# Performance work log

Measured on AMD Instinct MI355X. Metric: run time of the kernel, lower is better.

The kernel has to match this reference:

```python
import jax, jax.numpy as jnp
import numpy as np

SIZE = 1 << 24          # number of leaves (power of two, so bound == SIZE)
BOUND = 1 << 24         # padded power-of-two bound, as in SegmentTree.__init__
LOG2_BOUND = 24         # tree depth; traversal runs exactly this many steps
BATCH = 65536           # number of sampled prefix values


def setup_inputs() -> dict:
    key = jax.random.key(0)
    k1, k2 = jax.random.split(key)
    # leaf priorities must be non-negative (docstring warning for prefix-sum query)
    leaf = jax.random.uniform(k1, (SIZE,), dtype=jnp.float32)
    # fractions in [0,1); scaled by the root sum inside reference
    value_frac = jax.random.uniform(k2, (BATCH,), dtype=jnp.float32)
    return {"leaf": leaf, "value_frac": value_frac}


def _build_tree(leaf):
    """Bottom-up sums: heap layout, tree[1] = root, leaves at tree[BOUND:2*BOUND].
    Equivalent to repeated _setitem parent updates, done level-by-level (vectorized)."""
    levels = [leaf]
    lvl = leaf
    for _ in range(LOG2_BOUND):
        lvl = lvl.reshape(-1, 2).sum(axis=1)  # parent = left + right
        levels.append(lvl)
    # index 0 is an unused dummy slot (heap is 1-indexed)
    return jnp.concatenate([jnp.zeros((1,), leaf.dtype)] + levels[::-1])


def reference(leaf, value_frac):
    tree = _build_tree(leaf)
    # sampled prefix-sum targets in [0, root_sum)
    value = value_frac * tree[1]
    # faithful translation of _get_prefix_sum_idx: root-to-leaf binary descent.
    # The torch while-loop runs exactly log2(bound) iterations (index: 1 -> bound),
    # so a static Python loop is the jit-friendly equivalent.
    index = jnp.ones(value.shape, dtype=jnp.int32)  # 2*BOUND < 2^31, int32 safe
    for _ in range(LOG2_BOUND):
        index = index * 2
        lsons = tree[index]            # left-child subtree sums (gather)
        direct = lsons < value         # go right if left subtree too small
        value = value - lsons * direct
        index = index + direct
    index = index - BOUND              # convert heap position to leaf index
    priorities = leaf[index]           # priority of the sampled leaves
    return index, priorities
```

## Files before the change

kernel.cpp:

```cpp
#include <hip/hip_runtime.h>


#define BATCH_N 65536

#define OFF_ROOT 0
#define OFF_A 16
#define OFF_B 32
#define OFF_C 288
#define OFF_D 4384
#define OFF_E 69920

__device__ __forceinline__ float sum16_exact(float4 A, float4 B, float4 C, float4 D) {
    float n0 = A.x + A.y, n1 = A.z + A.w, n2 = B.x + B.y, n3 = B.z + B.w;
    float n4 = C.x + C.y, n5 = C.z + C.w, n6 = D.x + D.y, n7 = D.z + D.w;
    float m0 = n0 + n1, m1 = n2 + n3, m2 = n4 + n5, m3 = n6 + n7;
    return (m0 + m1) + (m2 + m3);
}

__device__ __forceinline__ float sum16_exact_s(const float* __restrict__ x) {
    float n0 = x[0] + x[1],  n1 = x[2] + x[3],  n2 = x[4] + x[5],  n3 = x[6] + x[7];
    float n4 = x[8] + x[9],  n5 = x[10] + x[11], n6 = x[12] + x[13], n7 = x[14] + x[15];
    float m0 = n0 + n1, m1 = n2 + n3, m2 = n4 + n5, m3 = n6 + n7;
    return (m0 + m1) + (m2 + m3);
}

__global__ __launch_bounds__(256) void build_lo(const float* __restrict__ leaf,
                                                float* __restrict__ ws) {
    __shared__ float smE[256];
    __shared__ float smD[16];
    const int t = threadIdx.x;
    const int b = blockIdx.x;
    const size_t gid = (size_t)b * 256 + t;
    const float4* q = reinterpret_cast<const float4*>(leaf) + gid * 4;
    float4 A = q[0], Bv = q[1], Cv = q[2], Dv = q[3];
    float e = sum16_exact(A, Bv, Cv, Dv);
    ws[OFF_E + gid] = e;
    smE[t] = e;
    __syncthreads();
    if (t < 16) {
        float d = sum16_exact_s(&smE[16 * t]);
        ws[OFF_D + (size_t)b * 16 + t] = d;
        smD[t] = d;
    }
    __syncthreads();
    if (t == 0) {
        ws[OFF_C + b] = sum16_exact_s(smD);
    }
}

__global__ __launch_bounds__(256) void build_top(float* __restrict__ ws) {
    __shared__ float smB[256];
    __shared__ float smA[16];
    const int t = threadIdx.x;
    const float4* q = reinterpret_cast<const float4*>(ws + OFF_C) + (size_t)t * 4;
    float4 A = q[0], Bv = q[1], Cv = q[2], Dv = q[3];
    float bnode = sum16_exact(A, Bv, Cv, Dv);
    ws[OFF_B + t] = bnode;
    smB[t] = bnode;
    __syncthreads();
    if (t < 16) {
        float anode = sum16_exact_s(&smB[16 * t]);
        ws[OFF_A + t] = anode;
        smA[t] = anode;
    }
    __syncthreads();
    if (t == 0) {
        ws[OFF_ROOT] = sum16_exact_s(smA);
    }
}

__device__ __forceinline__ void step16(const float* __restrict__ base, int& p, float& v,
                                       float& picked) {
    const float4* q = reinterpret_cast<const float4*>(base + (size_t)p * 16);
    float4 A = q[0], B = q[1], C = q[2], D = q[3];
    float n0 = A.x + A.y, n2 = B.x + B.y, n4 = C.x + C.y, n6 = D.x + D.y;
    float m0 = n0 + (A.z + A.w);
    float m2 = n4 + (C.z + C.w);
    float t0 = m0 + (n2 + (B.z + B.w));

    int ia = t0 < v;  if (ia) v -= t0;
    float mm = ia ? m2 : m0;
    int ib = mm < v;  if (ib) v -= mm;
    float nn = ia ? (ib ? n6 : n4) : (ib ? n2 : n0);
    int ic = nn < v;  if (ic) v -= nn;
    float se0 = ia ? C.x : A.x, se1 = ia ? C.z : A.z;
    float se2 = ia ? D.x : B.x, se3 = ia ? D.z : B.z;
    float so0 = ia ? C.y : A.y, so1 = ia ? C.w : A.w;
    float so2 = ia ? D.y : B.y, so3 = ia ? D.w : B.w;
    float ce = ic ? (ib ? se3 : se1) : (ib ? se2 : se0);
    float co = ic ? (ib ? so3 : so1) : (ib ? so2 : so0);
    int id = ce < v;  if (id) v -= ce;
    picked = id ? co : ce;
    p = p * 16 + ia * 8 + ib * 4 + ic * 2 + id;
}

__global__ __launch_bounds__(256) void descend(const float* __restrict__ leaf,
                                               const float* __restrict__ frac,
                                               const float* __restrict__ ws,
                                               float* __restrict__ out) {
    const int tid = blockIdx.x * 256 + threadIdx.x;
    float v = frac[tid] * ws[OFF_ROOT];
    int p = 0;
    float picked = 0.0f;
    step16(ws + OFF_A, p, v, picked);
    step16(ws + OFF_B, p, v, picked);
    step16(ws + OFF_C, p, v, picked);
    step16(ws + OFF_D, p, v, picked);
    step16(ws + OFF_E, p, v, picked);
    step16(leaf,       p, v, picked);
    out[tid] = (float)p;
    out[BATCH_N + tid] = picked;
}

extern "C" void kernel_launch(void* const* d_in, const int* in_sizes, int n_in,
                              void* d_out, int out_size, void* d_ws, size_t ws_size,
                              hipStream_t stream) {
    const float* leaf = (const float*)d_in[0];
    const float* frac = (const float*)d_in[1];
    float* out = (float*)d_out;
    float* ws  = (float*)d_ws;

    hipLaunchKernelGGL(build_lo,  dim3(4096), dim3(256), 0, stream, leaf, ws);
    hipLaunchKernelGGL(build_top, dim3(1),    dim3(256), 0, stream, ws);
    hipLaunchKernelGGL(descend,   dim3(256),  dim3(256), 0, stream, leaf, frac, ws, out);
}
```

Before: 97.98 us.

## Switch to 32-ary tree and fold top-level build into descend kernel

Replaces the 16-ary summary tree with a 32-ary one, so build_lo writes only two summary levels and descent needs fewer gather steps. The separate single-block build_top launch is removed; every descend block instead recomputes the top levels (C, B, root) from the D level into shared memory before traversing. This drops one kernel launch and one dependency-serialized tiny kernel, but every block redundantly reads the 64 KB D level, and each descent step now loads 128 bytes per node instead of 64.

```diff
diff --git a/kernel.cpp b/kernel.cpp
--- a/kernel.cpp
+++ b/kernel.cpp
@@ -3,111 +3,156 @@
 
 #define BATCH_N 65536
 
-#define OFF_ROOT 0
-#define OFF_A 16
-#define OFF_B 32
-#define OFF_C 288
-#define OFF_D 4384
-#define OFF_E 69920
+#define OFF_E 0
+#define OFF_D 524288
 
-__device__ __forceinline__ float sum16_exact(float4 A, float4 B, float4 C, float4 D) {
-    float n0 = A.x + A.y, n1 = A.z + A.w, n2 = B.x + B.y, n3 = B.z + B.w;
-    float n4 = C.x + C.y, n5 = C.z + C.w, n6 = D.x + D.y, n7 = D.z + D.w;
-    float m0 = n0 + n1, m1 = n2 + n3, m2 = n4 + n5, m3 = n6 + n7;
-    return (m0 + m1) + (m2 + m3);
-}
+#define C_STRIDE 36
 
-__device__ __forceinline__ float sum16_exact_s(const float* __restrict__ x) {
-    float n0 = x[0] + x[1],  n1 = x[2] + x[3],  n2 = x[4] + x[5],  n3 = x[6] + x[7];
-    float n4 = x[8] + x[9],  n5 = x[10] + x[11], n6 = x[12] + x[13], n7 = x[14] + x[15];
-    float m0 = n0 + n1, m1 = n2 + n3, m2 = n4 + n5, m3 = n6 + n7;
-    return (m0 + m1) + (m2 + m3);
+__device__ __forceinline__ float sum32_exact_s(const float* __restrict__ x) {
+    float n[16], m[8], p[4];
+#pragma unroll
+    for (int i = 0; i < 16; ++i) n[i] = x[2*i] + x[2*i+1];
+#pragma unroll
+    for (int i = 0; i < 8; ++i) m[i] = n[2*i] + n[2*i+1];
+#pragma unroll
+    for (int i = 0; i < 4; ++i) p[i] = m[2*i] + m[2*i+1];
+    return (p[0] + p[1]) + (p[2] + p[3]);
 }
 
 __global__ __launch_bounds__(256) void build_lo(const float* __restrict__ leaf,
                                                 float* __restrict__ ws) {
     __shared__ float smE[256];
-    __shared__ float smD[16];
     const int t = threadIdx.x;
     const int b = blockIdx.x;
     const size_t gid = (size_t)b * 256 + t;
-    const float4* q = reinterpret_cast<const float4*>(leaf) + gid * 4;
-    float4 A = q[0], Bv = q[1], Cv = q[2], Dv = q[3];
-    float e = sum16_exact(A, Bv, Cv, Dv);
+    const float4* q = reinterpret_cast<const float4*>(leaf) + gid * 8;
+    float c[32];
+#pragma unroll
+    for (int k = 0; k < 8; ++k) {
+        float4 v4 = q[k];
+        c[4*k+0] = v4.x; c[4*k+1] = v4.y; c[4*k+2] = v4.z; c[4*k+3] = v4.w;
+    }
+    float e = sum32_exact_s(c);
     ws[OFF_E + gid] = e;
     smE[t] = e;
     __syncthreads();
-    if (t < 16) {
-        float d = sum16_exact_s(&smE[16 * t]);
-        ws[OFF_D + (size_t)b * 16 + t] = d;
-        smD[t] = d;
-    }
-    __syncthreads();
-    if (t == 0) {
-        ws[OFF_C + b] = sum16_exact_s(smD);
+    if (t < 8) {
+        float d = sum32_exact_s(&smE[32 * t]);
+        ws[OFF_D + (size_t)b * 8 + t] = d;
     }
 }
 
-__global__ __launch_bounds__(256) void build_top(float* __restrict__ ws) {
-    __shared__ float smB[256];
-    __shared__ float smA[16];
-    const int t = threadIdx.x;
-    const float4* q = reinterpret_cast<const float4*>(ws + OFF_C) + (size_t)t * 4;
-    float4 A = q[0], Bv = q[1], Cv = q[2], Dv = q[3];
-    float bnode = sum16_exact(A, Bv, Cv, Dv);
-    ws[OFF_B + t] = bnode;
-    smB[t] = bnode;
-    __syncthreads();
-    if (t < 16) {
-        float anode = sum16_exact_s(&smB[16 * t]);
-        ws[OFF_A + t] = anode;
-        smA[t] = anode;
+template <int STRIDE>
+__device__ __forceinline__ void step32(const float* __restrict__ base, int& p, float& v,
+                                       float& picked) {
+    const float* node = base + (size_t)p * STRIDE;
+    float c[32];
+#pragma unroll
+    for (int k = 0; k < 8; ++k) {
+        float4 v4 = reinterpret_cast<const float4*>(node)[k];
+        c[4*k+0] = v4.x; c[4*k+1] = v4.y; c[4*k+2] = v4.z; c[4*k+3] = v4.w;
     }
-    __syncthreads();
-    if (t == 0) {
-        ws[OFF_ROOT] = sum16_exact_s(smA);
-    }
-}
+    float n[16], m[8], P[4];
+#pragma unroll
+    for (int i = 0; i < 16; ++i) n[i] = c[2*i] + c[2*i+1];
+#pragma unroll
+    for (int i = 0; i < 8; ++i) m[i] = n[2*i] + n[2*i+1];
+#pragma unroll
+    for (int i = 0; i < 4; ++i) P[i] = m[2*i] + m[2*i+1];
+    float q0 = P[0] + P[1];
 
-__device__ __forceinline__ void step16(const float* __restrict__ base, int& p, float& v,
-                                       float& picked) {
-    const float4* q = reinterpret_cast<const float4*>(base + (size_t)p * 16);
-    float4 A = q[0], B = q[1], C = q[2], D = q[3];
-    float n0 = A.x + A.y, n2 = B.x + B.y, n4 = C.x + C.y, n6 = D.x + D.y;
-    float m0 = n0 + (A.z + A.w);
-    float m2 = n4 + (C.z + C.w);
-    float t0 = m0 + (n2 + (B.z + B.w));
-
-    int ia = t0 < v;  if (ia) v -= t0;
-    float mm = ia ? m2 : m0;
-    int ib = mm < v;  if (ib) v -= mm;
-    float nn = ia ? (ib ? n6 : n4) : (ib ? n2 : n0);
-    int ic = nn < v;  if (ic) v -= nn;
-    float se0 = ia ? C.x : A.x, se1 = ia ? C.z : A.z;
-    float se2 = ia ? D.x : B.x, se3 = ia ? D.z : B.z;
-    float so0 = ia ? C.y : A.y, so1 = ia ? C.w : A.w;
-    float so2 = ia ? D.y : B.y, so3 = ia ? D.w : B.w;
-    float ce = ic ? (ib ? se3 : se1) : (ib ? se2 : se0);
-    float co = ic ? (ib ? so3 : so1) : (ib ? so2 : so0);
-    int id = ce < v;  if (id) v -= ce;
-    picked = id ? co : ce;
-    p = p * 16 + ia * 8 + ib * 4 + ic * 2 + id;
+    int ia = q0 < v;  if (ia) v -= q0;
+    float pp = ia ? P[2] : P[0];
+    int ib = pp < v;  if (ib) v -= pp;
+    float mm = ia ? (ib ? m[6] : m[4]) : (ib ? m[2] : m[0]);
+    int ic = mm < v;  if (ic) v -= mm;
+    float na = ib ? (ic ? n[6]  : n[4])  : (ic ? n[2]  : n[0]);
+    float nb = ib ? (ic ? n[14] : n[12]) : (ic ? n[10] : n[8]);
+    float nn = ia ? nb : na;
+    int id = nn < v;  if (id) v -= nn;
+    float e0 = id ? c[2]  : c[0],  e1 = id ? c[6]  : c[4];
+    float e2 = id ? c[10] : c[8],  e3 = id ? c[14] : c[12];
+    float e4 = id ? c[18] : c[16], e5 = id ? c[22] : c[20];
+    float e6 = id ? c[26] : c[24], e7 = id ? c[30] : c[28];
+    float f0 = ic ? e1 : e0, f1 = ic ? e3 : e2, f2 = ic ? e5 : e4, f3 = ic ? e7 : e6;
+    float g0 = ib ? f1 : f0, g1 = ib ? f3 : f2;
+    float ce = ia ? g1 : g0;
+    float o0 = id ? c[3]  : c[1],  o1 = id ? c[7]  : c[5];
+    float o2 = id ? c[11] : c[9],  o3 = id ? c[15] : c[13];
+    float o4 = id ? c[19] : c[17], o5 = id ? c[23] : c[21];
+    float o6 = id ? c[27] : c[25], o7 = id ? c[31] : c[29];
+    float h0 = ic ? o1 : o0, h1 = ic ? o3 : o2, h2 = ic ? o5 : o4, h3 = ic ? o7 : o6;
+    float k0 = ib ? h1 : h0, k1 = ib ? h3 : h2;
+    float co = ia ? k1 : k0;
+    int ie = ce < v;  if (ie) v -= ce;
+    picked = ie ? co : ce;
+    p = p * 32 + ia * 16 + ib * 8 + ic * 4 + id * 2 + ie;
 }
 
 __global__ __launch_bounds__(256) void descend(const float* __restrict__ leaf,
                                                const float* __restrict__ frac,
                                                const float* __restrict__ ws,
                                                float* __restrict__ out) {
-    const int tid = blockIdx.x * 256 + threadIdx.x;
-    float v = frac[tid] * ws[OFF_ROOT];
-    int p = 0;
+    __shared__ float smC[16 * C_STRIDE];
+    __shared__ float smB[16];
+    __shared__ float smRoot;
+    const int t = threadIdx.x;
+    const float* D = ws + OFF_D;
+
+#pragma unroll
+    for (int r = 0; r < 2; ++r) {
+        int j = t + r * 256;
+        const float4* q = reinterpret_cast<const float4*>(D) + (size_t)j * 8;
+        float c[32];
+#pragma unroll
+        for (int k = 0; k < 8; ++k) {
+            float4 v4 = q[k];
+            c[4*k+0] = v4.x; c[4*k+1] = v4.y; c[4*k+2] = v4.z; c[4*k+3] = v4.w;
+        }
+        smC[(j >> 5) * C_STRIDE + (j & 31)] = sum32_exact_s(c);
+    }
+    __syncthreads();
+    if (t < 16) {
+        smB[t] = sum32_exact_s(&smC[t * C_STRIDE]);
+    }
+    __syncthreads();
+    if (t == 0) {
+        float x[16];
+#pragma unroll
+        for (int i = 0; i < 16; ++i) x[i] = smB[i];
+        float n0 = x[0]+x[1], n1 = x[2]+x[3], n2 = x[4]+x[5], n3 = x[6]+x[7];
+        float n4 = x[8]+x[9], n5 = x[10]+x[11], n6 = x[12]+x[13], n7 = x[14]+x[15];
+        smRoot = ((n0+n1)+(n2+n3)) + ((n4+n5)+(n6+n7));
+    }
+    __syncthreads();
+
+    const int tid = blockIdx.x * 256 + t;
+    float v = frac[tid] * smRoot;
     float picked = 0.0f;
-    step16(ws + OFF_A, p, v, picked);
-    step16(ws + OFF_B, p, v, picked);
-    step16(ws + OFF_C, p, v, picked);
-    step16(ws + OFF_D, p, v, picked);
-    step16(ws + OFF_E, p, v, picked);
-    step16(leaf,       p, v, picked);
+
+    float x0 = smB[0],  x1 = smB[1],  x2 = smB[2],  x3 = smB[3];
+    float x4 = smB[4],  x5 = smB[5],  x6 = smB[6],  x7 = smB[7];
+    float x8 = smB[8],  x9 = smB[9],  xa = smB[10], xb = smB[11];
+    float xc = smB[12], xd = smB[13], xe = smB[14], xf = smB[15];
+    float n0 = x0+x1, n2 = x4+x5, n4 = x8+x9, n6 = xc+xd;
+    float m0 = n0 + (x2+x3);
+    float m2 = n4 + (xa+xb);
+    float t0 = m0 + (n2 + (x6+x7));
+    int ia = t0 < v;  if (ia) v -= t0;
+    float mm = ia ? m2 : m0;
+    int ib = mm < v;  if (ib) v -= mm;
+    float nn = ia ? (ib ? n6 : n4) : (ib ? n2 : n0);
+    int ic = nn < v;  if (ic) v -= nn;
+    float se = ia ? (ib ? (ic ? xe : xc) : (ic ? xa : x8))
+                  : (ib ? (ic ? x6 : x4) : (ic ? x2 : x0));
+    int id = se < v;  if (id) v -= se;
+    int p = ia * 8 + ib * 4 + ic * 2 + id;
+
+    step32<C_STRIDE>(smC,        p, v, picked);
+    step32<32>(ws + OFF_D,       p, v, picked);
+    step32<32>(ws + OFF_E,       p, v, picked);
+    step32<32>(leaf,             p, v, picked);
+
     out[tid] = (float)p;
     out[BATCH_N + tid] = picked;
 }
@@ -120,7 +165,6 @@
     float* out = (float*)d_out;
     float* ws  = (float*)d_ws;
 
-    hipLaunchKernelGGL(build_lo,  dim3(4096), dim3(256), 0, stream, leaf, ws);
-    hipLaunchKernelGGL(build_top, dim3(1),    dim3(256), 0, stream, ws);
-    hipLaunchKernelGGL(descend,   dim3(256),  dim3(256), 0, stream, leaf, frac, ws, out);
+    hipLaunchKernelGGL(build_lo, dim3(2048), dim3(256), 0, stream, leaf, ws);
+    hipLaunchKernelGGL(descend,  dim3(256),  dim3(256), 0, stream, leaf, frac, ws, out);
 }
```

Measured after the change: 100.2 us. +2.2%, slower.
